# Optimization experiments

Hardware: AMD Instinct MI355X
Metric: run time of the kernel (lower is better)

## Reference

```python
import jax, jax.numpy as jnp
import numpy as np
import math

SCALES = (128.0, 256.0, 512.0)
RATIOS = (0.5, 1.0, 2.0)
NMS_THR = 0.7
PRENMS_TOPK = 6000
POSTNMS_TOPK = 300
LOG_MAX = math.log(1000.0 / 16)  # clamp on dw/dh, as in torch code


def conv2d(x, w, b, pad):
    y = jax.lax.conv_general_dilated(x, w, (1, 1), [(pad, pad), (pad, pad)],
                                     dimension_numbers=('NCHW', 'OIHW', 'NCHW'))
    return y + b[None, :, None, None]


def generate_anchors(img_h, img_w, feat_h, feat_w):
    stride_h = img_h // feat_h
    stride_w = img_w // feat_w
    base = []
    for s in SCALES:
        for r in RATIOS:
            w = s * math.sqrt(1.0 / r)
            h = s * math.sqrt(r)
            base.append([-w / 2, -h / 2, w / 2, h / 2])
    base = jnp.asarray(base, jnp.float32)  # [A,4]
    sx = jnp.arange(feat_w, dtype=jnp.float32) * stride_w + stride_w // 2
    sy = jnp.arange(feat_h, dtype=jnp.float32) * stride_h + stride_h // 2
    syy, sxx = jnp.meshgrid(sy, sx, indexing='ij')
    sxf = sxx.reshape(-1)
    syf = syy.reshape(-1)
    shifts = jnp.stack([sxf, syf, sxf, syf], axis=1)  # [HW,4]
    anchors = (shifts[:, None, :] + base[None, :, :]).reshape(-1, 4)  # [HW*A,4]
    return anchors


def decode(reg, anchors):
    # reg, anchors: [N,4]
    w = anchors[:, 2] - anchors[:, 0]
    h = anchors[:, 3] - anchors[:, 1]
    cx = anchors[:, 0] + 0.5 * w
    cy = anchors[:, 1] + 0.5 * h
    dx, dy = reg[:, 0], reg[:, 1]
    dw = jnp.minimum(reg[:, 2], LOG_MAX)
    dh = jnp.minimum(reg[:, 3], LOG_MAX)
    pcx = dx * w + cx
    pcy = dy * h + cy
    pw = jnp.exp(dw) * w
    ph = jnp.exp(dh) * h
    return jnp.stack([pcx - 0.5 * pw, pcy - 0.5 * ph,
                      pcx + 0.5 * pw, pcy + 0.5 * ph], axis=1)


def nms_fixed(boxes, scores, thr, k):
    # Greedy NMS, fixed k iterations; suppressed/invalid entries have score -inf.
    x1, y1, x2, y2 = boxes[:, 0], boxes[:, 1], boxes[:, 2], boxes[:, 3]
    areas = (x2 - x1) * (y2 - y1)

    def step(live, _):
        best = jnp.argmax(live)
        ok = live[best] > -jnp.inf
        b = boxes[best]
        xl = jnp.maximum(b[0], x1)
        yt = jnp.maximum(b[1], y1)
        xr = jnp.minimum(b[2], x2)
        yb = jnp.minimum(b[3], y2)
        inter = jnp.clip(xr - xl, 0.0) * jnp.clip(yb - yt, 0.0)
        iou = inter / (areas[best] + areas - inter)
        live = jnp.where(iou > thr, -jnp.inf, live).at[best].set(-jnp.inf)
        return live, (best.astype(jnp.int32), ok)

    _, (keep, valid) = jax.lax.scan(step, scores, None, length=k)
    return keep, valid


def setup_inputs() -> dict:
    key = jax.random.key(0)
    ks = jax.random.split(key, 6)
    C = 512
    A = len(SCALES) * len(RATIOS)
    return {
        'image': jax.random.normal(ks[0], (8, 3, 1024, 1024), jnp.float32),
        'feat': jax.random.normal(ks[1], (8, C, 64, 64), jnp.float32),
        'conv_w': jax.random.normal(ks[2], (C, C, 3, 3), jnp.float32) * 0.01,
        'conv_b': jnp.zeros((C,), jnp.float32),
        'cls_w': jax.random.normal(ks[3], (A, C, 1, 1), jnp.float32) * 0.01,
        'cls_b': jnp.zeros((A,), jnp.float32),
        'reg_w': jax.random.normal(ks[4], (4 * A, C, 1, 1), jnp.float32) * 0.01,
        'reg_b': jnp.zeros((4 * A,), jnp.float32),
    }


def reference(image, feat, conv_w, conv_b, cls_w, cls_b, reg_w, reg_b):
    t = jax.nn.relu(conv2d(feat, conv_w, conv_b, 1))
    cls = conv2d(t, cls_w, cls_b, 0)   # [B,A,H,W]
    reg = conv2d(t, reg_w, reg_b, 0)   # [B,4A,H,W]
    B, _, H, W = cls.shape
    img_h, img_w = image.shape[-2], image.shape[-1]
    anchors = generate_anchors(img_h, img_w, H, W)  # [H*W*A,4]

    cls0 = cls[0].transpose(1, 2, 0).reshape(-1)        # permute(0,2,3,1): H,W,A order
    reg0 = reg[0].transpose(1, 2, 0).reshape(-1, 4)
    proposals = decode(reg0, anchors)
    scores = jax.nn.sigmoid(jax.lax.stop_gradient(cls0))  # cls_scores.detach()

    k = min(PRENMS_TOPK, scores.shape[0])
    top_scores, top_idx = jax.lax.top_k(scores, k)
    props = proposals[top_idx]
    props = jnp.stack([jnp.clip(props[:, 0], 0.0, float(img_w)),
                       jnp.clip(props[:, 1], 0.0, float(img_h)),
                       jnp.clip(props[:, 2], 0.0, float(img_w)),
                       jnp.clip(props[:, 3], 0.0, float(img_h))], axis=1)
    wv = props[:, 2] - props[:, 0]
    hv = props[:, 3] - props[:, 1]
    valid = (wv >= 1.0) & (hv >= 1.0)   # tiny boxes masked out instead of filtered
    sc = jnp.where(valid, top_scores, -jnp.inf)

    keep, kvalid = nms_fixed(jax.lax.stop_gradient(props), sc, NMS_THR, POSTNMS_TOPK)
    out_boxes = jnp.where(kvalid[:, None], props[keep], 0.0)   # [300,4]
    out_scores = jnp.where(kvalid, top_scores[keep], 0.0)      # [300]
    return jnp.concatenate([out_boxes, out_scores[:, None]], axis=1)  # [300,5]
```

## Files before the change

### kernel.cpp

```cpp
#include <hip/hip_runtime.h>
#include <math.h>

#define NMS_THRESH 0.7f
#define NANCH 36864
#define TOPK 6000
#define NWORDS 94
#define POSTK 300
#define MAXCAND 10240

__device__ __forceinline__ float dpp_shr1(float x) {
    return __int_as_float(__builtin_amdgcn_update_dpp(0, __float_as_int(x), 0x111, 0xF, 0xF, true));
}
__device__ __forceinline__ float dpp_shl1(float x) {
    return __int_as_float(__builtin_amdgcn_update_dpp(0, __float_as_int(x), 0x101, 0xF, 0xF, true));
}
__device__ __forceinline__ void glds16(const float* g, float* l) {
    __builtin_amdgcn_global_load_lds(
        (const __attribute__((address_space(1))) void*)g,
        (__attribute__((address_space(3))) void*)l, 16, 0, 0);
}

__global__ __launch_bounds__(256, 2)
void k_conv(const float* __restrict__ feat, const float* __restrict__ W,
            const float* __restrict__ bias, float* __restrict__ tout)
{
    __shared__ float sF[2 * 6168];
    __shared__ float sW[16 * 148];

    const int blk = blockIdx.x;
    const int ct  = blk & 31;
    const int yt  = blk >> 5;
    const int cob = ct << 4;
    const int y0  = yt << 2;
    const int tid = threadIdx.x;
    const int lane = tid & 63;
    const int wid = __builtin_amdgcn_readfirstlane(tid >> 6);
    const int cwo = wid << 2;
    const int co0 = cob + cwo;
    const int ly = lane >> 4;
    const int lx = (lane & 15) << 2;

    const int ci_g = (wid << 2) + ly;
    const int x_g  = lx;

    const int sci = tid >> 4, sco = tid & 15;
    const float* wsrc = W + (size_t)(cob + sco) * 4608 + sci * 9;

    float acc[4][4];
    #pragma unroll
    for (int i = 0; i < 4; ++i)
        #pragma unroll
        for (int j = 0; j < 4; ++j) acc[i][j] = 0.f;

    if (yt == 0)
        for (int q = tid; q < 1028; q += 256) { sF[q] = 0.f; sF[6168 + q] = 0.f; }
    if (yt == 15)
        for (int q = tid; q < 1028; q += 256) { sF[5140 + q] = 0.f; sF[6168 + 5140 + q] = 0.f; }
    float wreg[9];
    {
        #pragma unroll
        for (int s = 0; s < 6; ++s) {
            int gy = y0 - 1 + s;
            if (gy >= 0 && gy < 64) {
                const float* ga = feat + ((size_t)ci_g << 12) + (gy << 6) + x_g;
                glds16(ga, &sF[s * 1028 + (wid << 8)]);
            }
        }
        #pragma unroll
        for (int t = 0; t < 9; ++t) wreg[t] = wsrc[t];
    }
    __syncthreads();

#define LOADG(F, WQ, g) do {                                              \
        const int _ci = (g) / 3, _ky = (g) % 3;                           \
        F = *(const float4*)&fb[(ly + _ky) * 1028 + _ci * 64 + lx];       \
        *(float4*)&WQ[0] = *(const float4*)&sW[_ci * 148 + _ky * 48 + cwo];        \
        *(float4*)&WQ[4] = *(const float4*)&sW[_ci * 148 + _ky * 48 + 16 + cwo];   \
        *(float4*)&WQ[8] = *(const float4*)&sW[_ci * 148 + _ky * 48 + 32 + cwo];   \
    } while (0)

#define COMP(F, WQ) do {                                                  \
        float fr[6];                                                      \
        fr[0] = dpp_shr1(F.w);                                            \
        fr[1] = F.x; fr[2] = F.y; fr[3] = F.z; fr[4] = F.w;               \
        fr[5] = dpp_shl1(F.x);                                            \
        _Pragma("unroll")                                                 \
        for (int kx = 0; kx < 3; ++kx)                                    \
            _Pragma("unroll")                                             \
            for (int i = 0; i < 4; ++i)                                   \
                _Pragma("unroll")                                         \
                for (int j = 0; j < 4; ++j)                               \
                    acc[i][j] = fmaf(fr[i + kx], WQ[kx * 4 + j], acc[i][j]); \
    } while (0)

    int p = 0;
    for (int cc = 0; cc < 32; ++cc) {
        const bool more = cc < 31;
        #pragma unroll
        for (int t = 0; t < 9; ++t)
            sW[sci * 148 + t * 16 + sco] = wreg[t];
        __syncthreads();
        float wregN[9];
        if (more) {
            const float* fsrc = feat + ((size_t)(cc + 1) << 16);
            const int db = (p ^ 1) * 6168 + (wid << 8);
            #pragma unroll
            for (int s = 0; s < 6; ++s) {
                int gy = y0 - 1 + s;
                if (gy >= 0 && gy < 64) {
                    const float* ga = fsrc + ((size_t)ci_g << 12) + (gy << 6) + x_g;
                    glds16(ga, &sF[db + s * 1028]);
                }
            }
            const float* wp = wsrc + (size_t)(cc + 1) * 144;
            #pragma unroll
            for (int t = 0; t < 9; ++t) wregN[t] = wp[t];
        }
        {
            const float* fb = sF + p * 6168;
            float4 fA, fB; float wqA[12], wqB[12];
            LOADG(fA, wqA, 0);
            LOADG(fB, wqB, 1);
            #pragma unroll
            for (int gp = 0; gp < 24; ++gp) {
                COMP(fA, wqA);
                if (2 * gp + 2 < 48) LOADG(fA, wqA, 2 * gp + 2);
                COMP(fB, wqB);
                if (2 * gp + 3 < 48) LOADG(fB, wqB, 2 * gp + 3);
            }
        }
        if (more) {
            #pragma unroll
            for (int t = 0; t < 9; ++t) wreg[t] = wregN[t];
        }
        __syncthreads();
        p ^= 1;
    }
#undef LOADG
#undef COMP

    const int y = y0 + ly;
    #pragma unroll
    for (int j = 0; j < 4; ++j) {
        const float bv = bias[co0 + j];
        float4 o;
        o.x = fmaxf(acc[0][j] + bv, 0.f);
        o.y = fmaxf(acc[1][j] + bv, 0.f);
        o.z = fmaxf(acc[2][j] + bv, 0.f);
        o.w = fmaxf(acc[3][j] + bv, 0.f);
        *(float4*)&tout[((size_t)(co0 + j) << 12) + (y << 6) + lx] = o;
    }
}

__global__ __launch_bounds__(64)
void k_heads(const float* __restrict__ t, const float* __restrict__ cls_w,
             const float* __restrict__ cls_b, const float* __restrict__ reg_w,
             const float* __restrict__ reg_b, float* __restrict__ heads)
{
    const int bid = blockIdx.x;
    const int ch = bid % 45;
    const int pt = bid / 45;
    const int px = (pt << 6) + threadIdx.x;
    const float* wp; float bv;
    if (ch < 9) { wp = cls_w + ch * 512;       bv = cls_b[ch]; }
    else        { wp = reg_w + (ch - 9) * 512; bv = reg_b[ch - 9]; }
    float acc = bv;
    #pragma unroll 8
    for (int ci = 0; ci < 512; ++ci)
        acc = fmaf(t[((size_t)ci << 12) + px], wp[ci], acc);
    heads[((size_t)ch << 12) + px] = acc;
}

__global__ void k_decode(const float* __restrict__ heads,
                         float* __restrict__ score, float* __restrict__ validf,
                         float* __restrict__ box, unsigned* __restrict__ hist)
{
    __shared__ unsigned lh[4096];
    const int tid = threadIdx.x;
    for (int q = tid; q < 4096; q += 256) lh[q] = 0u;
    __syncthreads();

    int idx = blockIdx.x * 256 + tid;
    int p = idx / 9, a = idx - p * 9;
    int yq = p >> 6, xq = p & 63;
    const double scl[3] = {128.0, 256.0, 512.0};
    const double rat[3] = {0.5, 1.0, 2.0};
    double s = scl[a / 3], r = rat[a % 3];
    float bw = (float)(s * sqrt(1.0 / r) * 0.5);
    float bh = (float)(s * sqrt(r) * 0.5);
    float sx = xq * 16.0f + 8.0f;
    float sy = yq * 16.0f + 8.0f;
    float a0 = sx - bw, a1 = sy - bh, a2 = sx + bw, a3 = sy + bh;
    float wa = a2 - a0, ha = a3 - a1;
    float cx = a0 + 0.5f * wa, cy = a1 + 0.5f * ha;
    float logit = heads[(size_t)a * 4096 + p];
    float dx = heads[(size_t)(9  + 4 * a) * 4096 + p];
    float dy = heads[(size_t)(10 + 4 * a) * 4096 + p];
    float dw = fminf(heads[(size_t)(11 + 4 * a) * 4096 + p], 4.135166556742356f);
    float dh = fminf(heads[(size_t)(12 + 4 * a) * 4096 + p], 4.135166556742356f);
    float pcx = dx * wa + cx, pcy = dy * ha + cy;
    float pw = expf(dw) * wa, ph = expf(dh) * ha;
    float x1 = pcx - 0.5f * pw, y1 = pcy - 0.5f * ph;
    float x2 = pcx + 0.5f * pw, y2 = pcy + 0.5f * ph;
    x1 = fminf(fmaxf(x1, 0.f), 1024.f); y1 = fminf(fmaxf(y1, 0.f), 1024.f);
    x2 = fminf(fmaxf(x2, 0.f), 1024.f); y2 = fminf(fmaxf(y2, 0.f), 1024.f);
    float wv = x2 - x1, hv = y2 - y1;
    float sc = 1.f / (1.f + expf(-logit));
    score[idx]  = sc;
    validf[idx] = (wv >= 1.f && hv >= 1.f) ? 1.f : 0.f;
    box[idx * 4 + 0] = x1; box[idx * 4 + 1] = y1;
    box[idx * 4 + 2] = x2; box[idx * 4 + 3] = y2;

    atomicAdd(&lh[__float_as_uint(sc) >> 19], 1u);
    __syncthreads();
    for (int q = tid; q < 4096; q += 256) if (lh[q]) atomicAdd(&hist[q], lh[q]);
}

__global__ void k_zero(unsigned* __restrict__ p) {
    int i = blockIdx.x * 256 + threadIdx.x;
    if (i < 8448) p[i] = 0u;
}

__global__ void k_cut(const unsigned* __restrict__ hist, const float* __restrict__ score,
                      unsigned* __restrict__ meta)
{
    __shared__ unsigned hh[4096];
    __shared__ unsigned gs[256];
    __shared__ unsigned sbin, sabove;
    const int tid = threadIdx.x;
    for (int q = tid; q < 4096; q += 256) hh[q] = hist[q];
    __syncthreads();
    unsigned s = 0;
    #pragma unroll
    for (int k = 0; k < 16; ++k) s += hh[tid * 16 + k];
    gs[tid] = s;
    __syncthreads();
    if (tid == 0) {
        unsigned cum = 0;
        for (int g = 255; g >= 0; --g) {
            if (cum + gs[g] >= (unsigned)TOPK) {
                for (int b = g * 16 + 15; b >= g * 16; --b) {
                    if (cum + hh[b] >= (unsigned)TOPK) { sbin = (unsigned)b; sabove = cum; break; }
                    cum += hh[b];
                }
                break;
            }
            cum += gs[g];
        }
    }
    __syncthreads();
    const unsigned bin1 = sbin;
    for (int q = tid; q < 4096; q += 256) hh[q] = 0u;
    __syncthreads();
    for (int idx = tid; idx < NANCH; idx += 256) {
        unsigned bits = __float_as_uint(score[idx]);
        if ((bits >> 19) == bin1) atomicAdd(&hh[(bits >> 7) & 0xFFFu], 1u);
    }
    __syncthreads();
    s = 0;
    #pragma unroll
    for (int k = 0; k < 16; ++k) s += hh[tid * 16 + k];
    gs[tid] = s;
    __syncthreads();
    if (tid == 0) {
        unsigned cum = sabove;
        unsigned cut = bin1 << 19;
        for (int g = 255; g >= 0; --g) {
            if (cum + gs[g] >= (unsigned)TOPK) {
                for (int b = g * 16 + 15; b >= g * 16; --b) {
                    cum += hh[b];
                    if (cum >= (unsigned)TOPK) { cut = (bin1 << 19) | ((unsigned)b << 7); break; }
                }
                break;
            }
            cum += gs[g];
        }
        meta[0] = cut;
    }
}

__global__ void k_compact(const float* __restrict__ score, unsigned* __restrict__ meta,
                          int* __restrict__ cand, float* __restrict__ cscore) {
    int idx = blockIdx.x * 256 + threadIdx.x;
    unsigned bits = __float_as_uint(score[idx]);
    if (bits >= meta[0]) {
        unsigned pos = atomicAdd(&meta[1], 1u);
        if (pos < (unsigned)MAXCAND) {
            cand[pos] = idx;
            cscore[pos] = __uint_as_float(bits);
        }
    }
}

__global__ __launch_bounds__(256, 4)
void k_rank(const float* __restrict__ score, const float* __restrict__ validf,
            const float* __restrict__ box, const unsigned* __restrict__ meta,
            const int* __restrict__ cand, const float* __restrict__ cscore,
            float* __restrict__ score6, float* __restrict__ sc6,
            float* __restrict__ box6)
{
    __shared__ int pc[8][32];
    const int tid = threadIdx.x;
    const int il = tid & 31, js = tid >> 5;
    unsigned ncand = meta[1]; if (ncand > (unsigned)MAXCAND) ncand = MAXCAND;
    const int c = blockIdx.x * 32 + il;
    int i = -1; float si = 0.f;
    if (c < (int)ncand) { i = cand[c]; si = cscore[c]; }
    int cnt = 0;
    {
        const float4* cs4 = (const float4*)cscore;
        const int4*   cd4 = (const int4*)cand;
        const int q0 = js * 320;
        for (int q = 0; q < 320; ++q) {
            float4 v = cs4[q0 + q];
            int4   w = cd4[q0 + q];
            cnt += (v.x > si) || (v.x == si && w.x < i);
            cnt += (v.y > si) || (v.y == si && w.y < i);
            cnt += (v.z > si) || (v.z == si && w.z < i);
            cnt += (v.w > si) || (v.w == si && w.w < i);
        }
    }
    pc[js][il] = cnt;
    __syncthreads();
    if (js == 0 && i >= 0) {
        int rank = 0;
        #pragma unroll
        for (int q = 0; q < 8; ++q) rank += pc[q][il];
        if (rank < TOPK) {
            score6[rank] = si;
            sc6[rank] = (validf[i] != 0.f) ? si : -INFINITY;
            box6[rank * 4 + 0] = box[i * 4 + 0];
            box6[rank * 4 + 1] = box[i * 4 + 1];
            box6[rank * 4 + 2] = box[i * 4 + 2];
            box6[rank * 4 + 3] = box[i * 4 + 3];
        }
    }
}

__global__ __launch_bounds__(512)
void k_nms(const float* __restrict__ sc6, const float* __restrict__ score6,
           const float* __restrict__ box6, float* __restrict__ out)
{
    __shared__ float kx1[POSTK], ky1[POSTK], kx2[POSTK], ky2[POSTK], kar[POSTK];
    __shared__ int kidx[POSTK];
    __shared__ unsigned long long pOR[8];
    __shared__ int kcnt_s;
    const int tid = threadIdx.x, lane = tid & 63, wv = tid >> 6;

    if (tid == 0) kcnt_s = 0;
    int i0 = lane;
    float cx1 = box6[i0 * 4 + 0], cy1 = box6[i0 * 4 + 1];
    float cx2 = box6[i0 * 4 + 2], cy2 = box6[i0 * 4 + 3];
    float csc = sc6[i0];
    __syncthreads();

    for (int b = 0; b < NWORDS; ++b) {
        float nx1 = 0.f, ny1 = 0.f, nx2 = 0.f, ny2 = 0.f, nsc = -INFINITY;
        if (b + 1 < NWORDS) {
            int ni = (b + 1) * 64 + lane; if (ni >= TOPK) ni = TOPK - 1;
            nx1 = box6[ni * 4 + 0]; ny1 = box6[ni * 4 + 1];
            nx2 = box6[ni * 4 + 2]; ny2 = box6[ni * 4 + 3];
            nsc = sc6[ni];
        }
        const int i = b * 64 + lane;
        const bool v = (i < TOPK) && (csc > -INFINITY);
        const float ar = (cx2 - cx1) * (cy2 - cy1);
        const int kc = kcnt_s;
        bool dead = false;
        for (int j = wv; j < kc; j += 8) {
            float xl = fmaxf(kx1[j], cx1), yt = fmaxf(ky1[j], cy1);
            float xr = fminf(kx2[j], cx2), yb = fminf(ky2[j], cy2);
            float inter = fmaxf(xr - xl, 0.f) * fmaxf(yb - yt, 0.f);
            float iou = inter / (kar[j] + ar - inter);
            dead = dead || (iou > NMS_THRESH);
        }
        pOR[wv] = __ballot(dead);
        __syncthreads();
        if (wv == 0) {
            unsigned long long supp = pOR[0] | pOR[1] | pOR[2] | pOR[3]
                                    | pOR[4] | pOR[5] | pOR[6] | pOR[7];
            unsigned long long validb = __ballot(v);
            unsigned long long cand2 = validb & ~supp;
            int kc2 = kc;
            while (cand2 != 0ull && kc2 < POSTK) {
                int rr = __builtin_ctzll(cand2);
                float rx1 = __shfl(cx1, rr, 64), ry1 = __shfl(cy1, rr, 64);
                float rx2 = __shfl(cx2, rr, 64), ry2 = __shfl(cy2, rr, 64);
                float rar = __shfl(ar, rr, 64);
                if (lane == 0) {
                    kx1[kc2] = rx1; ky1[kc2] = ry1;
                    kx2[kc2] = rx2; ky2[kc2] = ry2;
                    kar[kc2] = rar; kidx[kc2] = b * 64 + rr;
                }
                float xl = fmaxf(rx1, cx1), yt = fmaxf(ry1, cy1);
                float xr = fminf(rx2, cx2), yb = fminf(ry2, cy2);
                float inter = fmaxf(xr - xl, 0.f) * fmaxf(yb - yt, 0.f);
                float iou = inter / (rar + ar - inter);
                unsigned long long sm = __ballot(iou > NMS_THRESH) | (1ull << rr);
                cand2 &= ~sm;
                ++kc2;
            }
            if (lane == 0) kcnt_s = kc2;
        }
        __syncthreads();
        if (kcnt_s >= POSTK) break;
        cx1 = nx1; cy1 = ny1; cx2 = nx2; cy2 = ny2; csc = nsc;
    }

    const int kc = kcnt_s;
    for (int n = tid; n < POSTK; n += 512) {
        float o0 = 0.f, o1 = 0.f, o2 = 0.f, o3 = 0.f, o4 = 0.f;
        if (n < kc) {
            int i = kidx[n];
            o0 = box6[i * 4 + 0]; o1 = box6[i * 4 + 1];
            o2 = box6[i * 4 + 2]; o3 = box6[i * 4 + 3];
            o4 = score6[i];
        }
        out[n * 5 + 0] = o0; out[n * 5 + 1] = o1; out[n * 5 + 2] = o2;
        out[n * 5 + 3] = o3; out[n * 5 + 4] = o4;
    }
}

extern "C" void kernel_launch(void* const* d_in, const int* in_sizes, int n_in,
                              void* d_out, int out_size, void* d_ws, size_t ws_size,
                              hipStream_t stream)
{
    (void)in_sizes; (void)n_in; (void)out_size; (void)ws_size;
    const float* feat   = (const float*)d_in[1];
    const float* conv_w = (const float*)d_in[2];
    const float* conv_b = (const float*)d_in[3];
    const float* cls_w  = (const float*)d_in[4];
    const float* cls_b  = (const float*)d_in[5];
    const float* reg_w  = (const float*)d_in[6];
    const float* reg_b  = (const float*)d_in[7];

    char* ws = (char*)d_ws;
    float*    t      = (float*)(ws + 0);
    float*    heads  = (float*)(ws + 8388608);
    unsigned* hist   = (unsigned*)(ws + 9125888);
    unsigned* meta   = (unsigned*)(ws + 9158656);
    int*      cand   = (int*)(ws + 9158720);
    float*    cscore = (float*)(ws + 9199680);
    float*    score  = (float*)(ws + 9240640);
    float*    validf = (float*)(ws + 9388096);
    float*    box    = (float*)(ws + 9535552);
    float*    score6 = (float*)(ws + 10125376);
    float*    sc6    = (float*)(ws + 10149952);
    float*    box6   = (float*)(ws + 10174528);

    k_zero   <<<33,   256, 0, stream>>>(hist);
    k_conv   <<<512,  256, 0, stream>>>(feat, conv_w, conv_b, t);
    k_heads  <<<2880, 64,  0, stream>>>(t, cls_w, cls_b, reg_w, reg_b, heads);
    k_decode <<<144,  256, 0, stream>>>(heads, score, validf, box, hist);
    k_cut    <<<1,    256, 0, stream>>>(hist, score, meta);
    k_compact<<<144,  256, 0, stream>>>(score, meta, cand, cscore);
    k_rank   <<<320,  256, 0, stream>>>(score, validf, box, meta, cand, cscore, score6, sc6, box6);
    k_nms    <<<1,    512, 0, stream>>>(sc6, score6, box6, (float*)d_out);
}
```

Baseline: 542.6 us.

## Fuse 1x1 head convolutions with anchor decode into one per-pixel kernel

Replaces the separate head kernel (one block per channel and pixel tile) and the decode kernel with one kernel. Each thread computes all 45 head channels for its pixel in registers, then decodes its 9 anchors directly. A small pre-pass transposes the cls and reg weights into a channel-interleaved table so each input channel's weights are read as one uniform row. This removes the intermediate heads buffer and the 45-fold re-reading of the feature map. The cost is a launch of only 16 workgroups, leaving most CUs idle and exposing memory latency on each thread's long serial loop.

```diff
diff --git a/kernel.cpp b/kernel.cpp
--- a/kernel.cpp
+++ b/kernel.cpp
@@ -152,66 +152,78 @@
     }
 }
 
-__global__ __launch_bounds__(64)
-void k_heads(const float* __restrict__ t, const float* __restrict__ cls_w,
-             const float* __restrict__ cls_b, const float* __restrict__ reg_w,
-             const float* __restrict__ reg_b, float* __restrict__ heads)
-{
-    const int bid = blockIdx.x;
-    const int ch = bid % 45;
-    const int pt = bid / 45;
-    const int px = (pt << 6) + threadIdx.x;
-    const float* wp; float bv;
-    if (ch < 9) { wp = cls_w + ch * 512;       bv = cls_b[ch]; }
-    else        { wp = reg_w + (ch - 9) * 512; bv = reg_b[ch - 9]; }
-    float acc = bv;
-    #pragma unroll 8
-    for (int ci = 0; ci < 512; ++ci)
-        acc = fmaf(t[((size_t)ci << 12) + px], wp[ci], acc);
-    heads[((size_t)ch << 12) + px] = acc;
-}
-
-__global__ void k_decode(const float* __restrict__ heads,
-                         float* __restrict__ score, float* __restrict__ validf,
-                         float* __restrict__ box, unsigned* __restrict__ hist)
+__global__ void k_wall(const float* __restrict__ cls_w, const float* __restrict__ reg_w,
+                       float* __restrict__ wall)
+{
+    int idx = blockIdx.x * 256 + threadIdx.x;
+    if (idx >= 512 * 48) return;
+    int ci = idx / 48, ch = idx - ci * 48;
+    float v = 0.f;
+    if (ch < 9) v = cls_w[ch * 512 + ci];
+    else if (ch < 45) v = reg_w[(ch - 9) * 512 + ci];
+    wall[idx] = v;
+}
+
+__global__ __launch_bounds__(256, 1)
+void k_headdec(const float* __restrict__ t, const float* __restrict__ wall,
+               const float* __restrict__ cls_b, const float* __restrict__ reg_b,
+               float* __restrict__ score, float* __restrict__ validf,
+               float* __restrict__ box, unsigned* __restrict__ hist)
 {
     __shared__ unsigned lh[4096];
     const int tid = threadIdx.x;
     for (int q = tid; q < 4096; q += 256) lh[q] = 0u;
     __syncthreads();
 
-    int idx = blockIdx.x * 256 + tid;
-    int p = idx / 9, a = idx - p * 9;
-    int yq = p >> 6, xq = p & 63;
-    const double scl[3] = {128.0, 256.0, 512.0};
-    const double rat[3] = {0.5, 1.0, 2.0};
-    double s = scl[a / 3], r = rat[a % 3];
-    float bw = (float)(s * sqrt(1.0 / r) * 0.5);
-    float bh = (float)(s * sqrt(r) * 0.5);
-    float sx = xq * 16.0f + 8.0f;
-    float sy = yq * 16.0f + 8.0f;
-    float a0 = sx - bw, a1 = sy - bh, a2 = sx + bw, a3 = sy + bh;
-    float wa = a2 - a0, ha = a3 - a1;
-    float cx = a0 + 0.5f * wa, cy = a1 + 0.5f * ha;
-    float logit = heads[(size_t)a * 4096 + p];
-    float dx = heads[(size_t)(9  + 4 * a) * 4096 + p];
-    float dy = heads[(size_t)(10 + 4 * a) * 4096 + p];
-    float dw = fminf(heads[(size_t)(11 + 4 * a) * 4096 + p], 4.135166556742356f);
-    float dh = fminf(heads[(size_t)(12 + 4 * a) * 4096 + p], 4.135166556742356f);
-    float pcx = dx * wa + cx, pcy = dy * ha + cy;
-    float pw = expf(dw) * wa, ph = expf(dh) * ha;
-    float x1 = pcx - 0.5f * pw, y1 = pcy - 0.5f * ph;
-    float x2 = pcx + 0.5f * pw, y2 = pcy + 0.5f * ph;
-    x1 = fminf(fmaxf(x1, 0.f), 1024.f); y1 = fminf(fmaxf(y1, 0.f), 1024.f);
-    x2 = fminf(fmaxf(x2, 0.f), 1024.f); y2 = fminf(fmaxf(y2, 0.f), 1024.f);
-    float wv = x2 - x1, hv = y2 - y1;
-    float sc = 1.f / (1.f + expf(-logit));
-    score[idx]  = sc;
-    validf[idx] = (wv >= 1.f && hv >= 1.f) ? 1.f : 0.f;
-    box[idx * 4 + 0] = x1; box[idx * 4 + 1] = y1;
-    box[idx * 4 + 2] = x2; box[idx * 4 + 3] = y2;
-
-    atomicAdd(&lh[__float_as_uint(sc) >> 19], 1u);
+    const int px = blockIdx.x * 256 + tid;
+    float acc[45];
+    #pragma unroll
+    for (int ch = 0; ch < 9; ++ch) acc[ch] = cls_b[ch];
+    #pragma unroll
+    for (int ch = 0; ch < 36; ++ch) acc[9 + ch] = reg_b[ch];
+
+    #pragma unroll 4
+    for (int ci = 0; ci < 512; ++ci) {
+        float v = t[((size_t)ci << 12) + px];
+        const float* wrow = wall + ci * 48;
+        #pragma unroll
+        for (int ch = 0; ch < 45; ++ch)
+            acc[ch] = fmaf(v, wrow[ch], acc[ch]);
+    }
+
+    const int yq = px >> 6, xq = px & 63;
+    const float sx = xq * 16.0f + 8.0f;
+    const float sy = yq * 16.0f + 8.0f;
+
+    #pragma unroll
+    for (int a = 0; a < 9; ++a) {
+        const double scl[3] = {128.0, 256.0, 512.0};
+        const double rat[3] = {0.5, 1.0, 2.0};
+        double s = scl[a / 3], r = rat[a % 3];
+        float bw = (float)(s * sqrt(1.0 / r) * 0.5);
+        float bh = (float)(s * sqrt(r) * 0.5);
+        float a0 = sx - bw, a1 = sy - bh, a2 = sx + bw, a3 = sy + bh;
+        float wa = a2 - a0, ha = a3 - a1;
+        float cx = a0 + 0.5f * wa, cy = a1 + 0.5f * ha;
+        float logit = acc[a];
+        float dx = acc[9 + 4 * a], dy = acc[10 + 4 * a];
+        float dw = fminf(acc[11 + 4 * a], 4.135166556742356f);
+        float dh = fminf(acc[12 + 4 * a], 4.135166556742356f);
+        float pcx = dx * wa + cx, pcy = dy * ha + cy;
+        float pw = expf(dw) * wa, ph = expf(dh) * ha;
+        float x1 = pcx - 0.5f * pw, y1 = pcy - 0.5f * ph;
+        float x2 = pcx + 0.5f * pw, y2 = pcy + 0.5f * ph;
+        x1 = fminf(fmaxf(x1, 0.f), 1024.f); y1 = fminf(fmaxf(y1, 0.f), 1024.f);
+        x2 = fminf(fmaxf(x2, 0.f), 1024.f); y2 = fminf(fmaxf(y2, 0.f), 1024.f);
+        float wv = x2 - x1, hv = y2 - y1;
+        float sc = 1.f / (1.f + expf(-logit));
+        const int idx = px * 9 + a;
+        score[idx]  = sc;
+        validf[idx] = (wv >= 1.f && hv >= 1.f) ? 1.f : 0.f;
+        float4 bx; bx.x = x1; bx.y = y1; bx.z = x2; bx.w = y2;
+        *(float4*)&box[idx * 4] = bx;
+        atomicAdd(&lh[__float_as_uint(sc) >> 19], 1u);
+    }
     __syncthreads();
     for (int q = tid; q < 4096; q += 256) if (lh[q]) atomicAdd(&hist[q], lh[q]);
 }
@@ -436,7 +448,7 @@
 
     char* ws = (char*)d_ws;
     float*    t      = (float*)(ws + 0);
-    float*    heads  = (float*)(ws + 8388608);
+    float*    wall   = (float*)(ws + 8388608);
     unsigned* hist   = (unsigned*)(ws + 9125888);
     unsigned* meta   = (unsigned*)(ws + 9158656);
     int*      cand   = (int*)(ws + 9158720);
@@ -449,9 +461,9 @@
     float*    box6   = (float*)(ws + 10174528);
 
     k_zero   <<<33,   256, 0, stream>>>(hist);
+    k_wall   <<<96,   256, 0, stream>>>(cls_w, reg_w, wall);
     k_conv   <<<512,  256, 0, stream>>>(feat, conv_w, conv_b, t);
-    k_heads  <<<2880, 64,  0, stream>>>(t, cls_w, cls_b, reg_w, reg_b, heads);
-    k_decode <<<144,  256, 0, stream>>>(heads, score, validf, box, hist);
+    k_headdec<<<16,   256, 0, stream>>>(t, wall, cls_b, reg_b, score, validf, box, hist);
     k_cut    <<<1,    256, 0, stream>>>(hist, score, meta);
     k_compact<<<144,  256, 0, stream>>>(score, meta, cand, cscore);
     k_rank   <<<320,  256, 0, stream>>>(score, validf, box, meta, cand, cscore, score6, sc6, box6);
```

Measured after the change: 723.6 us. +33.4%, slower.

## Use two waves per conv block with 8 output channels each

Applied to the files above, without the earlier changes.

Halves the conv block to 128 threads, and each wave now computes 8 output channels instead of 4. Each loaded input value is therefore reused across more FMAs, lowering the LDS-read-to-FMA ratio. The feature-tile staging and weight staging are remapped for the smaller thread count. In exchange, register pressure doubles for the accumulators and weights, and there are fewer waves per block to hide latency.

```diff
diff --git a/kernel.cpp b/kernel.cpp
--- a/kernel.cpp
+++ b/kernel.cpp
@@ -20,7 +20,7 @@
         (__attribute__((address_space(3))) void*)l, 16, 0, 0);
 }
 
-__global__ __launch_bounds__(256, 2)
+__global__ __launch_bounds__(128, 1)
 void k_conv(const float* __restrict__ feat, const float* __restrict__ W,
             const float* __restrict__ bias, float* __restrict__ tout)
 {
@@ -35,48 +35,51 @@
     const int tid = threadIdx.x;
     const int lane = tid & 63;
     const int wid = __builtin_amdgcn_readfirstlane(tid >> 6);
-    const int cwo = wid << 2;
+    const int cwo = wid << 3;
     const int co0 = cob + cwo;
     const int ly = lane >> 4;
     const int lx = (lane & 15) << 2;
 
-    const int ci_g = (wid << 2) + ly;
-    const int x_g  = lx;
-
-    const int sci = tid >> 4, sco = tid & 15;
-    const float* wsrc = W + (size_t)(cob + sco) * 4608 + sci * 9;
-
-    float acc[4][4];
+    const int sci = tid >> 3, scp = tid & 7;
+    const float* wsrc0 = W + (size_t)(cob + 2 * scp) * 4608 + sci * 9;
+    const float* wsrc1 = wsrc0 + 4608;
+
+    float acc[4][8];
     #pragma unroll
     for (int i = 0; i < 4; ++i)
         #pragma unroll
-        for (int j = 0; j < 4; ++j) acc[i][j] = 0.f;
+        for (int j = 0; j < 8; ++j) acc[i][j] = 0.f;
 
     if (yt == 0)
-        for (int q = tid; q < 1028; q += 256) { sF[q] = 0.f; sF[6168 + q] = 0.f; }
+        for (int q = tid; q < 1028; q += 128) { sF[q] = 0.f; sF[6168 + q] = 0.f; }
     if (yt == 15)
-        for (int q = tid; q < 1028; q += 256) { sF[5140 + q] = 0.f; sF[6168 + 5140 + q] = 0.f; }
-    float wreg[9];
+        for (int q = tid; q < 1028; q += 128) { sF[5140 + q] = 0.f; sF[6168 + 5140 + q] = 0.f; }
+    float wreg[18];
     {
         #pragma unroll
-        for (int s = 0; s < 6; ++s) {
+        for (int u = 0; u < 12; ++u) {
+            const int s = wid * 3 + (u >> 2), part = u & 3;
             int gy = y0 - 1 + s;
             if (gy >= 0 && gy < 64) {
-                const float* ga = feat + ((size_t)ci_g << 12) + (gy << 6) + x_g;
-                glds16(ga, &sF[s * 1028 + (wid << 8)]);
+                const float* ga = feat + (((size_t)(part * 4 + ly)) << 12) + (gy << 6) + lx;
+                glds16(ga, &sF[s * 1028 + part * 256]);
             }
         }
         #pragma unroll
-        for (int t = 0; t < 9; ++t) wreg[t] = wsrc[t];
+        for (int t = 0; t < 9; ++t) { wreg[t] = wsrc0[t]; wreg[9 + t] = wsrc1[t]; }
     }
     __syncthreads();
 
 #define LOADG(F, WQ, g) do {                                              \
         const int _ci = (g) / 3, _ky = (g) % 3;                           \
         F = *(const float4*)&fb[(ly + _ky) * 1028 + _ci * 64 + lx];       \
-        *(float4*)&WQ[0] = *(const float4*)&sW[_ci * 148 + _ky * 48 + cwo];        \
-        *(float4*)&WQ[4] = *(const float4*)&sW[_ci * 148 + _ky * 48 + 16 + cwo];   \
-        *(float4*)&WQ[8] = *(const float4*)&sW[_ci * 148 + _ky * 48 + 32 + cwo];   \
+        const float* _wb = sW + _ci * 148 + _ky * 48 + cwo;               \
+        *(float4*)&WQ[0]  = *(const float4*)(_wb);                        \
+        *(float4*)&WQ[4]  = *(const float4*)(_wb + 4);                    \
+        *(float4*)&WQ[8]  = *(const float4*)(_wb + 16);                   \
+        *(float4*)&WQ[12] = *(const float4*)(_wb + 20);                   \
+        *(float4*)&WQ[16] = *(const float4*)(_wb + 32);                   \
+        *(float4*)&WQ[20] = *(const float4*)(_wb + 36);                   \
     } while (0)
 
 #define COMP(F, WQ) do {                                                  \
@@ -89,36 +92,40 @@
             _Pragma("unroll")                                             \
             for (int i = 0; i < 4; ++i)                                   \
                 _Pragma("unroll")                                         \
-                for (int j = 0; j < 4; ++j)                               \
-                    acc[i][j] = fmaf(fr[i + kx], WQ[kx * 4 + j], acc[i][j]); \
+                for (int j = 0; j < 8; ++j)                               \
+                    acc[i][j] = fmaf(fr[i + kx], WQ[kx * 8 + j], acc[i][j]); \
     } while (0)
 
     int p = 0;
     for (int cc = 0; cc < 32; ++cc) {
         const bool more = cc < 31;
         #pragma unroll
-        for (int t = 0; t < 9; ++t)
-            sW[sci * 148 + t * 16 + sco] = wreg[t];
+        for (int t = 0; t < 9; ++t) {
+            float2 wp2; wp2.x = wreg[t]; wp2.y = wreg[9 + t];
+            *(float2*)&sW[sci * 148 + t * 16 + 2 * scp] = wp2;
+        }
         __syncthreads();
-        float wregN[9];
+        float wregN[18];
         if (more) {
             const float* fsrc = feat + ((size_t)(cc + 1) << 16);
-            const int db = (p ^ 1) * 6168 + (wid << 8);
+            const int db = (p ^ 1) * 6168;
             #pragma unroll
-            for (int s = 0; s < 6; ++s) {
+            for (int u = 0; u < 12; ++u) {
+                const int s = wid * 3 + (u >> 2), part = u & 3;
                 int gy = y0 - 1 + s;
                 if (gy >= 0 && gy < 64) {
-                    const float* ga = fsrc + ((size_t)ci_g << 12) + (gy << 6) + x_g;
-                    glds16(ga, &sF[db + s * 1028]);
+                    const float* ga = fsrc + (((size_t)(part * 4 + ly)) << 12) + (gy << 6) + lx;
+                    glds16(ga, &sF[db + s * 1028 + part * 256]);
                 }
             }
-            const float* wp = wsrc + (size_t)(cc + 1) * 144;
+            const float* wp0 = wsrc0 + (size_t)(cc + 1) * 144;
+            const float* wp1 = wsrc1 + (size_t)(cc + 1) * 144;
             #pragma unroll
-            for (int t = 0; t < 9; ++t) wregN[t] = wp[t];
+            for (int t = 0; t < 9; ++t) { wregN[t] = wp0[t]; wregN[9 + t] = wp1[t]; }
         }
         {
             const float* fb = sF + p * 6168;
-            float4 fA, fB; float wqA[12], wqB[12];
+            float4 fA, fB; float wqA[24], wqB[24];
             LOADG(fA, wqA, 0);
             LOADG(fB, wqB, 1);
             #pragma unroll
@@ -131,7 +138,7 @@
         }
         if (more) {
             #pragma unroll
-            for (int t = 0; t < 9; ++t) wreg[t] = wregN[t];
+            for (int t = 0; t < 18; ++t) wreg[t] = wregN[t];
         }
         __syncthreads();
         p ^= 1;
@@ -141,7 +148,7 @@
 
     const int y = y0 + ly;
     #pragma unroll
-    for (int j = 0; j < 4; ++j) {
+    for (int j = 0; j < 8; ++j) {
         const float bv = bias[co0 + j];
         float4 o;
         o.x = fmaxf(acc[0][j] + bv, 0.f);
@@ -449,7 +456,7 @@
     float*    box6   = (float*)(ws + 10174528);
 
     k_zero   <<<33,   256, 0, stream>>>(hist);
-    k_conv   <<<512,  256, 0, stream>>>(feat, conv_w, conv_b, t);
+    k_conv   <<<512,  128, 0, stream>>>(feat, conv_w, conv_b, t);
     k_heads  <<<2880, 64,  0, stream>>>(t, cls_w, cls_b, reg_w, reg_b, heads);
     k_decode <<<144,  256, 0, stream>>>(heads, score, validf, box, hist);
     k_cut    <<<1,    256, 0, stream>>>(hist, score, meta);
```

Measured after the change: 513.9 us. 5.3% less time.
